# Performance work log

Hardware: AMD Instinct MI355X
Metric: run time of the kernel (lower is better)

## Reference

```python
import jax, jax.numpy as jnp
import numpy as np

VOCAB = 32000   # vocab size
EDIM = 1024     # embedding dim
HDIM = 1024     # encoder hidden dim (fhid dim)
NACTS = 2       # ACTS = {'push': 0, 'pop': 1}
NCLASSES = 3
L = 256         # len_total
B = 128         # bsz
PAD = 0         # padding_idx
PUSH, POP = 0, 1


def setup_inputs() -> dict:
    key = jax.random.key(0)
    ks = jax.random.split(key, 10)

    def mk_seq(kt, kl):
        tok = jax.random.randint(kt, (L, B), 1, VOCAB)          # non-pad tokens
        lens = jax.random.randint(kl, (B,), L // 2, L - 1)      # ragged lengths
        t = jnp.arange(L)[:, None]
        # first lens+1 positions non-pad (so lens = L - n_pad - 1 as in the module)
        return jnp.where(t < lens[None, :] + 1, tok, PAD)

    seq1 = mk_seq(ks[0], ks[1])
    seq2 = mk_seq(ks[2], ks[3])

    def w(k, shp):
        return (jax.random.normal(k, shp, jnp.float32) * 0.02)

    return {
        "seq1": seq1, "seq2": seq2,
        "emb": w(ks[4], (VOCAB, EDIM)),
        "W_top": w(ks[5], (EDIM, HDIM)), "b_top": jnp.zeros((HDIM,), jnp.float32),
        "W_act": w(ks[6], (EDIM, NACTS)), "b_act": jnp.zeros((NACTS,), jnp.float32),
        "W1": w(ks[7], (4 * HDIM, HDIM)), "b1": jnp.zeros((HDIM,), jnp.float32),
        "W2": w(ks[8], (HDIM, NCLASSES)), "b2": jnp.zeros((NCLASSES,), jnp.float32),
    }


def _encode(seq, emb, W_top, b_top, W_act, b_act):
    # stub stack-encoder: time dim 2L-1 (one shift + one reduce step per token)
    seq_ext = jnp.concatenate([seq, seq[:-1]], axis=0)          # [2L-1, B]
    x = emb[seq_ext]                                            # [2L-1, B, E]
    top = jnp.tanh(jnp.einsum('tbe,eh->tbh', x, W_top) + b_top) # [2L-1, B, H]
    act = jax.nn.softmax(jnp.einsum('tbe,ea->tba', x, W_act) + b_act, axis=-1)
    return top, act


def _ragged_stats(act, Ts, bsz):
    # masked equivalents of the per-sample python loops over acts[:T, b, :]
    Tmax = act.shape[0]
    mask = (jnp.arange(Tmax)[:, None] < Ts[None, :]).astype(act.dtype)  # [2L-1, B]
    Tf = Ts.astype(act.dtype)
    push, pop = act[:, :, PUSH], act[:, :, POP]
    sum_push = (push * mask).sum(axis=0) / Tf                   # [B]
    sum_pop = ((pop * mask).sum(axis=0) + 1.0) / Tf             # [B]
    diff = jnp.sqrt((((push - pop) ** 2) * mask).sum(axis=0)) / Tf  # [B]
    dis = jnp.linalg.norm(sum_push - sum_pop) / bsz             # scalar
    return dis, diff.sum() / bsz


def reference(seq1, seq2, emb, W_top, b_top, W_act, b_act, W1, b1, W2, b2):
    bsz = seq1.shape[1]
    top1, act1 = _encode(seq1, emb, W_top, b_top, W_act, b_act)
    top2, act2 = _encode(seq2, emb, W_top, b_top, W_act, b_act)

    lens1 = seq1.shape[0] - (seq1 == PAD).sum(axis=0) - 1
    lens2 = seq2.shape[0] - (seq2 == PAD).sum(axis=0) - 1
    Ts1 = 2 * lens1 - 1
    Ts2 = 2 * lens2 - 1

    barange = jnp.arange(bsz)
    fhid1 = top1[Ts1 - 1, barange]                              # [B, H] ragged gather
    fhid2 = top2[Ts2 - 1, barange]

    u = jnp.concatenate([fhid1, fhid2, jnp.abs(fhid1 - fhid2), fhid1 * fhid2], axis=-1)
    res_clf = jax.nn.relu(u @ W1 + b1) @ W2 + b2                # [B, nclasses]

    dis1, diff1 = _ragged_stats(act1, Ts1, bsz)
    dis2, diff2 = _ragged_stats(act2, Ts2, bsz)
    return (res_clf, dis1, dis2, diff1, diff2)
```

## Files before the change

### kernel.cpp

```cpp
#include <hip/hip_runtime.h>
#include <math.h>

#define LL 256
#define BB 128
#define EDIM 1024
#define HDIM 1024
#define VOCAB 32000

#define NKSF 8
#define NKS  32

#define WS_EACT   0
#define WS_DELTA  32000
#define WS_DIFFB  32256
#define WS_TOKF   32512
#define WS_TS     32768
#define WS_FHID   33024
#define WS_BIG    295168

#define APAD 68

__device__ __forceinline__ void fma4(float4& a, float s, const float4& w) {
  a.x = fmaf(s, w.x, a.x); a.y = fmaf(s, w.y, a.y);
  a.z = fmaf(s, w.z, a.z); a.w = fmaf(s, w.w, a.w);
}

extern "C" __global__ __launch_bounds__(256)
void k_prep(const int* __restrict__ seq1, const int* __restrict__ seq2,
            int* __restrict__ tokf, int* __restrict__ Tsv) {
  int bx = blockIdx.x, tid = threadIdx.x;
  int s = bx >> 7, b = bx & 127;
  const int* seq = s ? seq2 : seq1;
  __shared__ int col[LL];
  __shared__ int red[256];
  int v = seq[tid * BB + b];
  col[tid] = v;
  red[tid] = (v == 0) ? 1 : 0;
  __syncthreads();
  for (int off = 128; off; off >>= 1) {
    if (tid < off) red[tid] += red[tid + off];
    __syncthreads();
  }
  if (tid == 0) {
    int lens = LL - red[0] - 1;
    int Ts = 2 * lens - 1;
    Tsv[bx] = Ts;
    int tt = Ts - 1;
    tokf[bx] = (tt < LL) ? col[tt] : col[tt - LL];
  }
}

extern "C" __global__ __launch_bounds__(256)
void k_fh_eact(const float* __restrict__ emb, const float* __restrict__ Wtop,
               const float* __restrict__ Wact, const int* __restrict__ tokf,
               float* __restrict__ fpart, float* __restrict__ Eact) {
  __shared__ float ash[128 * APAD];
  __shared__ int stok[128];
  int blk = blockIdx.x, tid = threadIdx.x;
  if (blk >= 256) {
    int lane = tid & 63, wave = tid >> 6;
    int v = (blk - 256) * 4 + wave;
    const float4* row = (const float4*)(emb + (size_t)v * EDIM);
    const float4* w4 = (const float4*)Wact;
    float a0 = 0.f;
#pragma unroll
    for (int it = 0; it < 4; ++it) {
      int i = lane + it * 64;
      float4 x = row[i];
      float4 wa = w4[2 * i];
      float4 wb = w4[2 * i + 1];
      a0 = fmaf(x.x, wa.x - wa.y, a0);
      a0 = fmaf(x.y, wa.z - wa.w, a0);
      a0 = fmaf(x.z, wb.x - wb.y, a0);
      a0 = fmaf(x.w, wb.z - wb.w, a0);
    }
#pragma unroll
    for (int off = 32; off; off >>= 1)
      a0 += __shfl_down(a0, off, 64);
    if (lane == 0) Eact[v] = a0;
    return;
  }
  int ks = blk >> 5, rb = (blk >> 4) & 1, cb = blk & 15;
  int cg = tid & 15, rgr = tid >> 4;
  int c0 = cb * 64 + cg * 4;
  int kbase = ks * 128;
  if (tid < 128) stok[tid] = tokf[rb * 128 + tid];
  float4 acc[8];
#pragma unroll
  for (int r = 0; r < 8; ++r) acc[r] = make_float4(0.f, 0.f, 0.f, 0.f);
#pragma unroll
  for (int ch = 0; ch < 2; ++ch) {
    int kg = kbase + ch * 64;
    __syncthreads();
    for (int idx = tid; idx < 128 * 16; idx += 256) {
      int r = idx >> 4, q = idx & 15;
      *(float4*)&ash[r * APAD + q * 4] =
          ((const float4*)(emb + (size_t)stok[r] * EDIM + kg))[q];
    }
    __syncthreads();
    const float* Wp = Wtop + (size_t)kg * HDIM + c0;
    float4 w[4];
#pragma unroll
    for (int j = 0; j < 4; ++j) w[j] = *(const float4*)(Wp + (size_t)j * HDIM);
#pragma unroll
    for (int kk = 0; kk < 64; kk += 4) {
      float4 wn[4];
      if (kk + 4 < 64) {
#pragma unroll
        for (int j = 0; j < 4; ++j) wn[j] = *(const float4*)(Wp + (size_t)(kk + 4 + j) * HDIM);
      }
#pragma unroll
      for (int r = 0; r < 8; ++r) {
        float4 a = *(const float4*)&ash[(rgr * 8 + r) * APAD + kk];
        fma4(acc[r], a.x, w[0]); fma4(acc[r], a.y, w[1]);
        fma4(acc[r], a.z, w[2]); fma4(acc[r], a.w, w[3]);
      }
#pragma unroll
      for (int j = 0; j < 4; ++j) w[j] = wn[j];
    }
  }
  float* dst = fpart + ((size_t)ks * 256 + rb * 128 + rgr * 8) * HDIM + c0;
#pragma unroll
  for (int r = 0; r < 8; ++r)
    *(float4*)(dst + (size_t)r * HDIM) = acc[r];
}

extern "C" __global__ __launch_bounds__(256)
void k_ftanh(const float* __restrict__ fpart, const float* __restrict__ btop,
             float* __restrict__ fhid) {
  int g = blockIdx.x * 256 + threadIdx.x;
  float4 s = ((const float4*)fpart)[g];
#pragma unroll
  for (int k = 1; k < NKSF; ++k) {
    float4 p = ((const float4*)fpart)[(size_t)k * 65536 + g];
    s.x += p.x; s.y += p.y; s.z += p.z; s.w += p.w;
  }
  float4 b = ((const float4*)btop)[g & 255];
  ((float4*)fhid)[g] = make_float4(tanhf(s.x + b.x), tanhf(s.y + b.y),
                                   tanhf(s.z + b.z), tanhf(s.w + b.w));
}

extern "C" __global__ __launch_bounds__(256)
void k_part_stats(const float* __restrict__ fhid, const float* __restrict__ W1,
                  const int* __restrict__ seq1, const int* __restrict__ seq2,
                  const float* __restrict__ Eact, const float* __restrict__ b_act,
                  const int* __restrict__ Tsv,
                  float* __restrict__ part, float* __restrict__ delta,
                  float* __restrict__ diffb) {
  __shared__ float ush[128 * APAD];
  int blk = blockIdx.x, tid = threadIdx.x;
  if (blk >= 512) {
    int sb = blk - 512;
    int s = sb >> 7, b = sb & 127;
    const int* seq = s ? seq2 : seq1;
    int* col = (int*)ush;
    float* redf = ush + 256;
    col[tid] = seq[tid * BB + b];
    __syncthreads();
    int Ts = Tsv[sb];
    float ba = b_act[0] - b_act[1];
    float sp = 0.f, sq = 0.f;
    for (int t = tid; t < Ts; t += 256) {
      int tok = (t < LL) ? col[t] : col[t - LL];
      float d = Eact[tok] + ba;
      float p0 = 1.0f / (1.0f + expf(-d));
      float dd = 2.f * p0 - 1.f;
      sp += dd;
      sq = fmaf(dd, dd, sq);
    }
    redf[tid] = sp; __syncthreads();
    for (int off = 128; off; off >>= 1) { if (tid < off) redf[tid] += redf[tid + off]; __syncthreads(); }
    float tsp = redf[0]; __syncthreads();
    redf[tid] = sq; __syncthreads();
    for (int off = 128; off; off >>= 1) { if (tid < off) redf[tid] += redf[tid + off]; __syncthreads(); }
    if (tid == 0) {
      float Tf = (float)Ts;
      delta[sb] = (tsp - 1.0f) / Tf;
      diffb[sb] = sqrtf(redf[0]) / Tf;
    }
    return;
  }
  int ksb = blk >> 4, cb = blk & 15;
  int cg = tid & 15, rgr = tid >> 4;
  int c0 = cb * 64 + cg * 4;
  int kbase = ksb * 128;
  int seg = kbase >> 10;
  const float4* f4 = (const float4*)fhid;
  float4 acc[8];
#pragma unroll
  for (int r = 0; r < 8; ++r) acc[r] = make_float4(0.f, 0.f, 0.f, 0.f);
  float4 sreg[8];
#define GATHER(ch)                                                        \
  {                                                                       \
    int fb4 = ((kbase + (ch) * 64) & 1023) >> 2;                          \
    _Pragma("unroll")                                                     \
    for (int j = 0; j < 8; ++j) {                                         \
      int idx = tid + j * 256;                                            \
      int r = idx >> 4, q = idx & 15;                                     \
      float4 u;                                                           \
      if (seg == 0) u = f4[r * 256 + fb4 + q];                            \
      else if (seg == 1) u = f4[(128 + r) * 256 + fb4 + q];               \
      else {                                                              \
        float4 f1 = f4[r * 256 + fb4 + q];                                \
        float4 f2 = f4[(128 + r) * 256 + fb4 + q];                        \
        if (seg == 2)                                                     \
          u = make_float4(fabsf(f1.x - f2.x), fabsf(f1.y - f2.y),         \
                          fabsf(f1.z - f2.z), fabsf(f1.w - f2.w));        \
        else                                                              \
          u = make_float4(f1.x * f2.x, f1.y * f2.y, f1.z * f2.z, f1.w * f2.w); \
      }                                                                   \
      sreg[j] = u;                                                        \
    }                                                                     \
  }
  GATHER(0)
#pragma unroll
  for (int ch = 0; ch < 2; ++ch) {
    __syncthreads();
#pragma unroll
    for (int j = 0; j < 8; ++j) {
      int idx = tid + j * 256;
      int r = idx >> 4, q = idx & 15;
      *(float4*)&ush[r * APAD + q * 4] = sreg[j];
    }
    __syncthreads();
    if (ch == 0) GATHER(1)
    int kg = kbase + ch * 64;
    const float* Wp = W1 + (size_t)kg * HDIM + c0;
    float4 w[4];
#pragma unroll
    for (int j = 0; j < 4; ++j) w[j] = *(const float4*)(Wp + (size_t)j * HDIM);
#pragma unroll
    for (int kk = 0; kk < 64; kk += 4) {
      float4 wn[4];
      if (kk + 4 < 64) {
#pragma unroll
        for (int j = 0; j < 4; ++j) wn[j] = *(const float4*)(Wp + (size_t)(kk + 4 + j) * HDIM);
      }
#pragma unroll
      for (int r = 0; r < 8; ++r) {
        float4 a = *(const float4*)&ush[(rgr * 8 + r) * APAD + kk];
        fma4(acc[r], a.x, w[0]); fma4(acc[r], a.y, w[1]);
        fma4(acc[r], a.z, w[2]); fma4(acc[r], a.w, w[3]);
      }
#pragma unroll
      for (int j = 0; j < 4; ++j) w[j] = wn[j];
    }
  }
#undef GATHER
  float* dst = part + ((size_t)ksb * 128 + rgr * 8) * HDIM + c0;
#pragma unroll
  for (int r = 0; r < 8; ++r)
    *(float4*)(dst + (size_t)r * HDIM) = acc[r];
}

extern "C" __global__ __launch_bounds__(256)
void k_clf_final(const float* __restrict__ part, const float* __restrict__ b1,
                 const float* __restrict__ W2, const float* __restrict__ b2,
                 const float* __restrict__ delta, const float* __restrict__ diffb,
                 float* __restrict__ out) {
  int blk = blockIdx.x, tid = threadIdx.x;
  __shared__ float red[768];
  if (blk == 128) {
    for (int s = 0; s < 2; ++s) {
      float v = 0.f, w = 0.f;
      if (tid < BB) { float d = delta[s * BB + tid]; v = d * d; w = diffb[s * BB + tid]; }
      red[tid] = v; __syncthreads();
      for (int off = 128; off; off >>= 1) { if (tid < off) red[tid] += red[tid + off]; __syncthreads(); }
      if (tid == 0) out[384 + s] = sqrtf(red[0]) / (float)BB;
      __syncthreads();
      red[tid] = w; __syncthreads();
      for (int off = 128; off; off >>= 1) { if (tid < off) red[tid] += red[tid + off]; __syncthreads(); }
      if (tid == 0) out[386 + s] = red[0] / (float)BB;
      __syncthreads();
    }
    return;
  }
  int b = blk;
  float4 p = ((const float4*)b1)[tid];
  const float4* p4 = (const float4*)part;
#pragma unroll
  for (int ks = 0; ks < NKS; ++ks) {
    float4 q = p4[((size_t)ks * 128 + b) * 256 + tid];
    p.x += q.x; p.y += q.y; p.z += q.z; p.w += q.w;
  }
  p.x = fmaxf(p.x, 0.f); p.y = fmaxf(p.y, 0.f);
  p.z = fmaxf(p.z, 0.f); p.w = fmaxf(p.w, 0.f);
  int k0 = tid * 4;
  float a0 = 0.f, a1 = 0.f, a2 = 0.f;
  a0 = fmaf(p.x, W2[(k0 + 0) * 3 + 0], a0); a1 = fmaf(p.x, W2[(k0 + 0) * 3 + 1], a1); a2 = fmaf(p.x, W2[(k0 + 0) * 3 + 2], a2);
  a0 = fmaf(p.y, W2[(k0 + 1) * 3 + 0], a0); a1 = fmaf(p.y, W2[(k0 + 1) * 3 + 1], a1); a2 = fmaf(p.y, W2[(k0 + 1) * 3 + 2], a2);
  a0 = fmaf(p.z, W2[(k0 + 2) * 3 + 0], a0); a1 = fmaf(p.z, W2[(k0 + 2) * 3 + 1], a1); a2 = fmaf(p.z, W2[(k0 + 2) * 3 + 2], a2);
  a0 = fmaf(p.w, W2[(k0 + 3) * 3 + 0], a0); a1 = fmaf(p.w, W2[(k0 + 3) * 3 + 1], a1); a2 = fmaf(p.w, W2[(k0 + 3) * 3 + 2], a2);
  red[tid] = a0; red[256 + tid] = a1; red[512 + tid] = a2;
  __syncthreads();
  for (int off = 128; off; off >>= 1) {
    if (tid < off) {
      red[tid] += red[tid + off];
      red[256 + tid] += red[256 + tid + off];
      red[512 + tid] += red[512 + tid + off];
    }
    __syncthreads();
  }
  if (tid == 0) {
    out[b * 3 + 0] = red[0]   + b2[0];
    out[b * 3 + 1] = red[256] + b2[1];
    out[b * 3 + 2] = red[512] + b2[2];
  }
}

extern "C" void kernel_launch(void* const* d_in, const int* in_sizes, int n_in,
                              void* d_out, int out_size, void* d_ws, size_t ws_size,
                              hipStream_t stream) {
  const int*   seq1  = (const int*)  d_in[0];
  const int*   seq2  = (const int*)  d_in[1];
  const float* emb   = (const float*)d_in[2];
  const float* W_top = (const float*)d_in[3];
  const float* b_top = (const float*)d_in[4];
  const float* W_act = (const float*)d_in[5];
  const float* b_act = (const float*)d_in[6];
  const float* W1    = (const float*)d_in[7];
  const float* b1    = (const float*)d_in[8];
  const float* W2    = (const float*)d_in[9];
  const float* b2    = (const float*)d_in[10];
  float* out = (float*)d_out;
  float* ws  = (float*)d_ws;

  float* Eact  = ws + WS_EACT;
  float* delta = ws + WS_DELTA;
  float* diffb = ws + WS_DIFFB;
  int*   tokf  = (int*)(ws + WS_TOKF);
  int*   Tsv   = (int*)(ws + WS_TS);
  float* fhid  = ws + WS_FHID;
  float* bigb  = ws + WS_BIG;

  hipLaunchKernelGGL(k_prep,       dim3(256),        dim3(256), 0, stream, seq1, seq2, tokf, Tsv);
  hipLaunchKernelGGL(k_fh_eact,    dim3(256 + 8000), dim3(256), 0, stream, emb, W_top, W_act, tokf, bigb, Eact);
  hipLaunchKernelGGL(k_ftanh,      dim3(256),        dim3(256), 0, stream, bigb, b_top, fhid);
  hipLaunchKernelGGL(k_part_stats, dim3(768),        dim3(256), 0, stream, fhid, W1, seq1, seq2, Eact, b_act, Tsv, bigb, delta, diffb);
  hipLaunchKernelGGL(k_clf_final,  dim3(129),        dim3(256), 0, stream, bigb, b1, W2, b2, delta, diffb, out);
}
```

Measured before the change: 265.8 us.

## Drop prep kernel, recompute lengths inline, and split W1 GEMM finer

Removes the separate prep launch. Each GEMM block of the first kernel now counts padding itself to find its gather token. The ragged stats work moves into the tanh kernel, which recomputes Ts locally. The W1 partial GEMM now uses 64-wide K slices over 1024 blocks instead of two 64-chunks per block, which doubles the split-K partials reduced in the final kernel. This trades one fewer launch and more parallelism for redundant seq scans per block and more partial-sum traffic.

Measured after the change: 258.3 us, median of 2. 1.03x faster.

```diff
diff --git a/kernel.cpp b/kernel.cpp
--- a/kernel.cpp
+++ b/kernel.cpp
@@ -8,13 +8,11 @@
 #define VOCAB 32000
 
 #define NKSF 8
-#define NKS  32
+#define NKS  64
 
 #define WS_EACT   0
 #define WS_DELTA  32000
 #define WS_DIFFB  32256
-#define WS_TOKF   32512
-#define WS_TS     32768
 #define WS_FHID   33024
 #define WS_BIG    295168
 
@@ -26,33 +24,9 @@
 }
 
 extern "C" __global__ __launch_bounds__(256)
-void k_prep(const int* __restrict__ seq1, const int* __restrict__ seq2,
-            int* __restrict__ tokf, int* __restrict__ Tsv) {
-  int bx = blockIdx.x, tid = threadIdx.x;
-  int s = bx >> 7, b = bx & 127;
-  const int* seq = s ? seq2 : seq1;
-  __shared__ int col[LL];
-  __shared__ int red[256];
-  int v = seq[tid * BB + b];
-  col[tid] = v;
-  red[tid] = (v == 0) ? 1 : 0;
-  __syncthreads();
-  for (int off = 128; off; off >>= 1) {
-    if (tid < off) red[tid] += red[tid + off];
-    __syncthreads();
-  }
-  if (tid == 0) {
-    int lens = LL - red[0] - 1;
-    int Ts = 2 * lens - 1;
-    Tsv[bx] = Ts;
-    int tt = Ts - 1;
-    tokf[bx] = (tt < LL) ? col[tt] : col[tt - LL];
-  }
-}
-
-extern "C" __global__ __launch_bounds__(256)
 void k_fh_eact(const float* __restrict__ emb, const float* __restrict__ Wtop,
-               const float* __restrict__ Wact, const int* __restrict__ tokf,
+               const float* __restrict__ Wact,
+               const int* __restrict__ seq1, const int* __restrict__ seq2,
                float* __restrict__ fpart, float* __restrict__ Eact) {
   __shared__ float ash[128 * APAD];
   __shared__ int stok[128];
@@ -84,7 +58,21 @@
   int cg = tid & 15, rgr = tid >> 4;
   int c0 = cb * 64 + cg * 4;
   int kbase = ks * 128;
-  if (tid < 128) stok[tid] = tokf[rb * 128 + tid];
+  const int* seq = rb ? seq2 : seq1;
+  {
+    int c = tid >> 1, h = tid & 1;
+    int z = 0;
+    int base = h * 128;
+    for (int r = 0; r < 128; ++r)
+      z += (seq[(base + r) * BB + c] == 0) ? 1 : 0;
+    z += __shfl_xor(z, 1, 64);
+    if (h == 0) {
+      int lens = 255 - z;
+      int tt = 2 * lens - 2;
+      int idx = (tt < LL) ? tt : tt - LL;
+      stok[c] = seq[idx * BB + c];
+    }
+  }
   float4 acc[8];
 #pragma unroll
   for (int r = 0; r < 8; ++r) acc[r] = make_float4(0.f, 0.f, 0.f, 0.f);
@@ -126,127 +114,117 @@
 }
 
 extern "C" __global__ __launch_bounds__(256)
-void k_ftanh(const float* __restrict__ fpart, const float* __restrict__ btop,
-             float* __restrict__ fhid) {
-  int g = blockIdx.x * 256 + threadIdx.x;
-  float4 s = ((const float4*)fpart)[g];
-#pragma unroll
-  for (int k = 1; k < NKSF; ++k) {
-    float4 p = ((const float4*)fpart)[(size_t)k * 65536 + g];
-    s.x += p.x; s.y += p.y; s.z += p.z; s.w += p.w;
-  }
-  float4 b = ((const float4*)btop)[g & 255];
-  ((float4*)fhid)[g] = make_float4(tanhf(s.x + b.x), tanhf(s.y + b.y),
-                                   tanhf(s.z + b.z), tanhf(s.w + b.w));
+void k_ftanh_stats(const float* __restrict__ fpart, const float* __restrict__ btop,
+                   const int* __restrict__ seq1, const int* __restrict__ seq2,
+                   const float* __restrict__ Eact, const float* __restrict__ b_act,
+                   float* __restrict__ fhid, float* __restrict__ delta,
+                   float* __restrict__ diffb) {
+  int blk = blockIdx.x, tid = threadIdx.x;
+  if (blk < 256) {
+    int g = blk * 256 + tid;
+    float4 s = ((const float4*)fpart)[g];
+#pragma unroll
+    for (int k = 1; k < NKSF; ++k) {
+      float4 p = ((const float4*)fpart)[(size_t)k * 65536 + g];
+      s.x += p.x; s.y += p.y; s.z += p.z; s.w += p.w;
+    }
+    float4 b = ((const float4*)btop)[g & 255];
+    ((float4*)fhid)[g] = make_float4(tanhf(s.x + b.x), tanhf(s.y + b.y),
+                                     tanhf(s.z + b.z), tanhf(s.w + b.w));
+    return;
+  }
+  int sb = blk - 256;
+  int s = sb >> 7, b = sb & 127;
+  const int* seq = s ? seq2 : seq1;
+  __shared__ int col[LL];
+  __shared__ int zred[256];
+  __shared__ float redf[256];
+  int v = seq[tid * BB + b];
+  col[tid] = v;
+  zred[tid] = (v == 0) ? 1 : 0;
+  __syncthreads();
+  for (int off = 128; off; off >>= 1) {
+    if (tid < off) zred[tid] += zred[tid + off];
+    __syncthreads();
+  }
+  int lens = LL - zred[0] - 1;
+  int Ts = 2 * lens - 1;
+  float ba = b_act[0] - b_act[1];
+  float sp = 0.f, sq = 0.f;
+  for (int t = tid; t < Ts; t += 256) {
+    int tok = (t < LL) ? col[t] : col[t - LL];
+    float d = Eact[tok] + ba;
+    float p0 = 1.0f / (1.0f + expf(-d));
+    float dd = 2.f * p0 - 1.f;
+    sp += dd;
+    sq = fmaf(dd, dd, sq);
+  }
+  redf[tid] = sp; __syncthreads();
+  for (int off = 128; off; off >>= 1) { if (tid < off) redf[tid] += redf[tid + off]; __syncthreads(); }
+  float tsp = redf[0]; __syncthreads();
+  redf[tid] = sq; __syncthreads();
+  for (int off = 128; off; off >>= 1) { if (tid < off) redf[tid] += redf[tid + off]; __syncthreads(); }
+  if (tid == 0) {
+    float Tf = (float)Ts;
+    delta[sb] = (tsp - 1.0f) / Tf;
+    diffb[sb] = sqrtf(redf[0]) / Tf;
+  }
 }
 
 extern "C" __global__ __launch_bounds__(256)
-void k_part_stats(const float* __restrict__ fhid, const float* __restrict__ W1,
-                  const int* __restrict__ seq1, const int* __restrict__ seq2,
-                  const float* __restrict__ Eact, const float* __restrict__ b_act,
-                  const int* __restrict__ Tsv,
-                  float* __restrict__ part, float* __restrict__ delta,
-                  float* __restrict__ diffb) {
+void k_part(const float* __restrict__ fhid, const float* __restrict__ W1,
+            float* __restrict__ part) {
   __shared__ float ush[128 * APAD];
   int blk = blockIdx.x, tid = threadIdx.x;
-  if (blk >= 512) {
-    int sb = blk - 512;
-    int s = sb >> 7, b = sb & 127;
-    const int* seq = s ? seq2 : seq1;
-    int* col = (int*)ush;
-    float* redf = ush + 256;
-    col[tid] = seq[tid * BB + b];
-    __syncthreads();
-    int Ts = Tsv[sb];
-    float ba = b_act[0] - b_act[1];
-    float sp = 0.f, sq = 0.f;
-    for (int t = tid; t < Ts; t += 256) {
-      int tok = (t < LL) ? col[t] : col[t - LL];
-      float d = Eact[tok] + ba;
-      float p0 = 1.0f / (1.0f + expf(-d));
-      float dd = 2.f * p0 - 1.f;
-      sp += dd;
-      sq = fmaf(dd, dd, sq);
-    }
-    redf[tid] = sp; __syncthreads();
-    for (int off = 128; off; off >>= 1) { if (tid < off) redf[tid] += redf[tid + off]; __syncthreads(); }
-    float tsp = redf[0]; __syncthreads();
-    redf[tid] = sq; __syncthreads();
-    for (int off = 128; off; off >>= 1) { if (tid < off) redf[tid] += redf[tid + off]; __syncthreads(); }
-    if (tid == 0) {
-      float Tf = (float)Ts;
-      delta[sb] = (tsp - 1.0f) / Tf;
-      diffb[sb] = sqrtf(redf[0]) / Tf;
-    }
-    return;
-  }
   int ksb = blk >> 4, cb = blk & 15;
   int cg = tid & 15, rgr = tid >> 4;
   int c0 = cb * 64 + cg * 4;
-  int kbase = ksb * 128;
+  int kbase = ksb * 64;
   int seg = kbase >> 10;
+  int fb4 = (kbase & 1023) >> 2;
   const float4* f4 = (const float4*)fhid;
+#pragma unroll
+  for (int j = 0; j < 8; ++j) {
+    int idx = tid + j * 256;
+    int r = idx >> 4, q = idx & 15;
+    float4 u;
+    if (seg == 0) u = f4[r * 256 + fb4 + q];
+    else if (seg == 1) u = f4[(128 + r) * 256 + fb4 + q];
+    else {
+      float4 f1 = f4[r * 256 + fb4 + q];
+      float4 f2 = f4[(128 + r) * 256 + fb4 + q];
+      if (seg == 2)
+        u = make_float4(fabsf(f1.x - f2.x), fabsf(f1.y - f2.y),
+                        fabsf(f1.z - f2.z), fabsf(f1.w - f2.w));
+      else
+        u = make_float4(f1.x * f2.x, f1.y * f2.y, f1.z * f2.z, f1.w * f2.w);
+    }
+    *(float4*)&ush[r * APAD + q * 4] = u;
+  }
   float4 acc[8];
 #pragma unroll
   for (int r = 0; r < 8; ++r) acc[r] = make_float4(0.f, 0.f, 0.f, 0.f);
-  float4 sreg[8];
-#define GATHER(ch)                                                        \
-  {                                                                       \
-    int fb4 = ((kbase + (ch) * 64) & 1023) >> 2;                          \
-    _Pragma("unroll")                                                     \
-    for (int j = 0; j < 8; ++j) {                                         \
-      int idx = tid + j * 256;                                            \
-      int r = idx >> 4, q = idx & 15;                                     \
-      float4 u;                                                           \
-      if (seg == 0) u = f4[r * 256 + fb4 + q];                            \
-      else if (seg == 1) u = f4[(128 + r) * 256 + fb4 + q];               \
-      else {                                                              \
-        float4 f1 = f4[r * 256 + fb4 + q];                                \
-        float4 f2 = f4[(128 + r) * 256 + fb4 + q];                        \
-        if (seg == 2)                                                     \
-          u = make_float4(fabsf(f1.x - f2.x), fabsf(f1.y - f2.y),         \
-                          fabsf(f1.z - f2.z), fabsf(f1.w - f2.w));        \
-        else                                                              \
-          u = make_float4(f1.x * f2.x, f1.y * f2.y, f1.z * f2.z, f1.w * f2.w); \
-      }                                                                   \
-      sreg[j] = u;                                                        \
-    }                                                                     \
-  }
-  GATHER(0)
-#pragma unroll
-  for (int ch = 0; ch < 2; ++ch) {
-    __syncthreads();
-#pragma unroll
-    for (int j = 0; j < 8; ++j) {
-      int idx = tid + j * 256;
-      int r = idx >> 4, q = idx & 15;
-      *(float4*)&ush[r * APAD + q * 4] = sreg[j];
-    }
-    __syncthreads();
-    if (ch == 0) GATHER(1)
-    int kg = kbase + ch * 64;
-    const float* Wp = W1 + (size_t)kg * HDIM + c0;
-    float4 w[4];
-#pragma unroll
-    for (int j = 0; j < 4; ++j) w[j] = *(const float4*)(Wp + (size_t)j * HDIM);
-#pragma unroll
-    for (int kk = 0; kk < 64; kk += 4) {
-      float4 wn[4];
-      if (kk + 4 < 64) {
-#pragma unroll
-        for (int j = 0; j < 4; ++j) wn[j] = *(const float4*)(Wp + (size_t)(kk + 4 + j) * HDIM);
-      }
-#pragma unroll
-      for (int r = 0; r < 8; ++r) {
-        float4 a = *(const float4*)&ush[(rgr * 8 + r) * APAD + kk];
-        fma4(acc[r], a.x, w[0]); fma4(acc[r], a.y, w[1]);
-        fma4(acc[r], a.z, w[2]); fma4(acc[r], a.w, w[3]);
-      }
-#pragma unroll
-      for (int j = 0; j < 4; ++j) w[j] = wn[j];
-    }
-  }
-#undef GATHER
+  __syncthreads();
+  const float* Wp = W1 + (size_t)kbase * HDIM + c0;
+  float4 w[4];
+#pragma unroll
+  for (int j = 0; j < 4; ++j) w[j] = *(const float4*)(Wp + (size_t)j * HDIM);
+#pragma unroll
+  for (int kk = 0; kk < 64; kk += 4) {
+    float4 wn[4];
+    if (kk + 4 < 64) {
+#pragma unroll
+      for (int j = 0; j < 4; ++j) wn[j] = *(const float4*)(Wp + (size_t)(kk + 4 + j) * HDIM);
+    }
+#pragma unroll
+    for (int r = 0; r < 8; ++r) {
+      float4 a = *(const float4*)&ush[(rgr * 8 + r) * APAD + kk];
+      fma4(acc[r], a.x, w[0]); fma4(acc[r], a.y, w[1]);
+      fma4(acc[r], a.z, w[2]); fma4(acc[r], a.w, w[3]);
+    }
+#pragma unroll
+    for (int j = 0; j < 4; ++j) w[j] = wn[j];
+  }
   float* dst = part + ((size_t)ksb * 128 + rgr * 8) * HDIM + c0;
 #pragma unroll
   for (int r = 0; r < 8; ++r)
@@ -278,7 +256,6 @@
   int b = blk;
   float4 p = ((const float4*)b1)[tid];
   const float4* p4 = (const float4*)part;
-#pragma unroll
   for (int ks = 0; ks < NKS; ++ks) {
     float4 q = p4[((size_t)ks * 128 + b) * 256 + tid];
     p.x += q.x; p.y += q.y; p.z += q.z; p.w += q.w;
@@ -328,14 +305,11 @@
   float* Eact  = ws + WS_EACT;
   float* delta = ws + WS_DELTA;
   float* diffb = ws + WS_DIFFB;
-  int*   tokf  = (int*)(ws + WS_TOKF);
-  int*   Tsv   = (int*)(ws + WS_TS);
   float* fhid  = ws + WS_FHID;
   float* bigb  = ws + WS_BIG;
 
-  hipLaunchKernelGGL(k_prep,       dim3(256),        dim3(256), 0, stream, seq1, seq2, tokf, Tsv);
-  hipLaunchKernelGGL(k_fh_eact,    dim3(256 + 8000), dim3(256), 0, stream, emb, W_top, W_act, tokf, bigb, Eact);
-  hipLaunchKernelGGL(k_ftanh,      dim3(256),        dim3(256), 0, stream, bigb, b_top, fhid);
-  hipLaunchKernelGGL(k_part_stats, dim3(768),        dim3(256), 0, stream, fhid, W1, seq1, seq2, Eact, b_act, Tsv, bigb, delta, diffb);
-  hipLaunchKernelGGL(k_clf_final,  dim3(129),        dim3(256), 0, stream, bigb, b1, W2, b2, delta, diffb, out);
-}
+  hipLaunchKernelGGL(k_fh_eact,     dim3(256 + 8000), dim3(256), 0, stream, emb, W_top, W_act, seq1, seq2, bigb, Eact);
+  hipLaunchKernelGGL(k_ftanh_stats, dim3(512),        dim3(256), 0, stream, bigb, b_top, seq1, seq2, Eact, b_act, fhid, delta, diffb);
+  hipLaunchKernelGGL(k_part,        dim3(1024),       dim3(256), 0, stream, fhid, W1, bigb);
+  hipLaunchKernelGGL(k_clf_final,   dim3(129),        dim3(256), 0, stream, bigb, b1, W2, b2, delta, diffb, out);
+}
```
